# Kernel tuning notes

Measured on AMD Instinct MI355X. Metric: run time of the kernel, lower is better.

Reference implementation:

```python
import jax, jax.numpy as jnp
import numpy as np

N_NODES = 50000
N_EDGES = 1_600_000
IN_DIM = 256
OUT_DIM = 128
NEG_SLOPE = 0.01  # F.leaky_relu default


def setup_inputs() -> dict:
    key = jax.random.key(0)
    k1, k2, k3, k4, k5 = jax.random.split(key, 5)
    x = jax.random.normal(k1, (N_NODES, IN_DIM), dtype=jnp.float32)
    # glorot_init: uniform in [-r, r], r = sqrt(6/(in+out))
    r = np.sqrt(6.0 / (IN_DIM + OUT_DIM)).astype(np.float32)
    weight = jax.random.uniform(k2, (IN_DIM, OUT_DIM), dtype=jnp.float32, minval=-r, maxval=r)
    adj_rows = jax.random.randint(k3, (N_EDGES,), 0, N_NODES, dtype=jnp.int64 if jax.config.jax_enable_x64 else jnp.int32)
    adj_cols = jax.random.randint(k4, (N_EDGES,), 0, N_NODES, dtype=jnp.int64 if jax.config.jax_enable_x64 else jnp.int32)
    adj_vals = jax.random.uniform(k5, (N_EDGES,), dtype=jnp.float32)
    return {"x": x, "weight": weight, "adj_vals": adj_vals,
            "adj_rows": adj_rows, "adj_cols": adj_cols}


def reference(x, weight, adj_vals, adj_rows, adj_cols):
    # h = X @ W : [N, OUT_DIM]
    h = x @ weight
    # sparse adj @ h via edge-list SpMM: out[r] += v * h[c]
    msgs = adj_vals[:, None] * h[adj_cols]            # [E, OUT_DIM]
    agg = jax.ops.segment_sum(msgs, adj_rows, num_segments=N_NODES)
    # leaky_relu epilogue
    return jnp.where(agg >= 0, agg, NEG_SLOPE * agg)
```

## Files before the change

kernel.cpp:

```cpp
#include <hip/hip_runtime.h>
#include <hip/hip_fp16.h>

#define N_NODES 50000
#define N_EDGES 1600000
#define IN_DIM 256
#define OUT_DIM 128
#define NEG_SLOPE 0.01f

#define SB_SH     10
#define NSB       49
#define BIN_SH    4
#define BIN_ROWS  16
#define NBIN_PAD  (NSB * 64)
#define NPART     16
#define ECAP      2560
#define SEGP      96
#define CAPG      (NPART * SEGP)
#define OVF_CAP   65536

#define SCAT_BLOCKS 256
#define EPB_S (N_EDGES / SCAT_BLOCKS)
#define SCAT_ITERS ((EPB_S + 511) / 512)

#define BM 128
#define GEMM_BLOCKS ((N_NODES + BM - 1) / BM)
#define PREP_BLOCKS (SCAT_BLOCKS + GEMM_BLOCKS + 1)

typedef _Float16 f16x8 __attribute__((ext_vector_type(8)));
typedef float    f32x4 __attribute__((ext_vector_type(4)));
typedef float    f32x8 __attribute__((ext_vector_type(8)));

__device__ __forceinline__ float lrelu(float v) {
    return v >= 0.f ? v : NEG_SLOPE * v;
}

#define CVT16(lo, hi) do { \
    lo[0]=(_Float16)xr[0].x; lo[1]=(_Float16)xr[0].y; lo[2]=(_Float16)xr[0].z; lo[3]=(_Float16)xr[0].w; \
    lo[4]=(_Float16)xr[1].x; lo[5]=(_Float16)xr[1].y; lo[6]=(_Float16)xr[1].z; lo[7]=(_Float16)xr[1].w; \
    hi[0]=(_Float16)xr[2].x; hi[1]=(_Float16)xr[2].y; hi[2]=(_Float16)xr[2].z; hi[3]=(_Float16)xr[2].w; \
    hi[4]=(_Float16)xr[3].x; hi[5]=(_Float16)xr[3].y; hi[6]=(_Float16)xr[3].z; hi[7]=(_Float16)xr[3].w; \
} while (0)

__global__ __launch_bounds__(512, 2) void prep(const int* __restrict__ rows,
                                               const int* __restrict__ cols,
                                               const float* __restrict__ vals,
                                               const float* __restrict__ x,
                                               const float* __restrict__ w,
                                               int* __restrict__ cstartarr,
                                               int* __restrict__ ovfcnt,
                                               int2* __restrict__ cbuf,
                                               __half* __restrict__ h) {
    __shared__ __attribute__((aligned(16))) char smem[50432];
    const int bid = blockIdx.x;
    const int t   = threadIdx.x;

    if (bid >= SCAT_BLOCKS + GEMM_BLOCKS) {
        if (t == 0) *ovfcnt = 0;
        return;
    }

    if (bid < SCAT_BLOCKS) {
        int2* lsort  = (int2*)smem;
        int*  hist   = (int*)(smem + 50000);
        int*  cstart = (int*)(smem + 50200);
        const int lane  = t & 63;
        const int blk   = bid;
        const int ebase = blk * EPB_S;

        if (t < NSB) hist[t] = 0;
        __syncthreads();

        int myr[SCAT_ITERS];
#pragma unroll
        for (int k = 0; k < SCAT_ITERS; ++k) {
            const int i = k * 512 + t;
            myr[k] = -1;
            if (i < EPB_S) {
                myr[k] = rows[ebase + i];
                atomicAdd(&hist[myr[k] >> SB_SH], 1);
            }
        }
        __syncthreads();

        if (t < 64) {
            const int v = (t < NSB) ? hist[t] : 0;
            int s = v;
#pragma unroll
            for (int off = 1; off < 64; off <<= 1) {
                const int u = __shfl_up(s, off);
                if (lane >= off) s += u;
            }
            if (t < NSB) { cstart[t] = s - v; hist[t] = s - v; }
        }
        __syncthreads();

#pragma unroll
        for (int k = 0; k < SCAT_ITERS; ++k) {
            const int i = k * 512 + t;
            if (i < EPB_S) {
                const int e = ebase + i;
                const int r = myr[k];
                const int pos = atomicAdd(&hist[r >> SB_SH], 1);
                lsort[pos] = make_int2((int)(((unsigned)r << 16) | (unsigned)cols[e]),
                                       __float_as_int(vals[e]));
            }
        }
        __syncthreads();

        {
            const int4* src = (const int4*)lsort;
            int4* dst = (int4*)(cbuf + (size_t)blk * EPB_S);
            for (int i = t; i < EPB_S / 2; i += 512) dst[i] = src[i];
        }
        if (t < NSB)  cstartarr[blk * 50 + t]   = cstart[t];
        if (t == NSB) cstartarr[blk * 50 + NSB] = EPB_S;
        return;
    }

    f16x8* wt8h = (f16x8*)smem;
    f16x8* xs8  = (f16x8*)(smem + 32768);
    const int a256 = (t < 256);
    const int lane = t & 63;
    const int wv   = t >> 6;
    const int row0 = (bid - SCAT_BLOCKS) * BM;

    const int srow = t >> 1;
    const int skh  = t & 1;
    const int grow = row0 + srow;
    const bool rv  = a256 && (grow < N_NODES);
    const float* xp = x + (size_t)(rv ? grow : 0) * IN_DIM + skh * 16;

    float4 xr[4];
    if (a256) {
#pragma unroll
        for (int i = 0; i < 4; ++i)
            xr[i] = rv ? ((const float4*)xp)[i] : make_float4(0.f, 0.f, 0.f, 0.f);
        f16x8 lo, hi;
        CVT16(lo, hi);
        xs8[(0 * 4 + skh * 2 + 0) * 128 + srow] = lo;
        xs8[(0 * 4 + skh * 2 + 1) * 128 + srow] = hi;
    }
    __syncthreads();

    f32x4 acc[2][8];
#pragma unroll
    for (int mf = 0; mf < 2; ++mf)
#pragma unroll
        for (int nf = 0; nf < 8; ++nf) acc[mf][nf] = (f32x4){0.f, 0.f, 0.f, 0.f};

    const int kgl = lane >> 4;
    const int l15 = lane & 15;
    const int mb  = (wv << 5) + l15;

#pragma unroll
    for (int H = 0; H < 2; ++H) {
        if (a256) {
#pragma unroll
            for (int itr = 0; itr < 8; ++itr) {
                const int e  = itr * 2048 + t * 8;
                const int kl = e >> 7;
                const int n0 = e & 127;
                const float4 a4 = *(const float4*)(w + (size_t)((H << 7) + kl) * 128 + n0);
                const float4 b4 = *(const float4*)(w + (size_t)((H << 7) + kl) * 128 + n0 + 4);
                __half* d = (__half*)wt8h + (size_t)(((kl >> 3) << 7) + n0) * 8 + (kl & 7);
                d[0]  = __float2half(a4.x);
                d[8]  = __float2half(a4.y);
                d[16] = __float2half(a4.z);
                d[24] = __float2half(a4.w);
                d[32] = __float2half(b4.x);
                d[40] = __float2half(b4.y);
                d[48] = __float2half(b4.z);
                d[56] = __float2half(b4.w);
            }
        }
        __syncthreads();

#pragma unroll
        for (int ksl = 0; ksl < 4; ++ksl) {
            const int ks  = H * 4 + ksl;
            const int cur = ks & 1;
            if (a256 && ks < 7) {
#pragma unroll
                for (int i = 0; i < 4; ++i)
                    xr[i] = rv ? ((const float4*)(xp + (ks + 1) * 32))[i]
                               : make_float4(0.f, 0.f, 0.f, 0.f);
            }
            if (a256) {
                const f16x8 b0 = xs8[(cur * 4 + kgl) * 128 + mb];
                const f16x8 b1 = xs8[(cur * 4 + kgl) * 128 + mb + 16];
                const int abase = ((ksl * 4 + kgl) << 7) + l15;
#pragma unroll
                for (int nf = 0; nf < 8; ++nf) {
                    const f16x8 a = wt8h[abase + (nf << 4)];
                    acc[0][nf] = __builtin_amdgcn_mfma_f32_16x16x32_f16(a, b0, acc[0][nf], 0, 0, 0);
                    acc[1][nf] = __builtin_amdgcn_mfma_f32_16x16x32_f16(a, b1, acc[1][nf], 0, 0, 0);
                }
            }
            if (a256 && ks < 7) {
                f16x8 lo, hi;
                CVT16(lo, hi);
                xs8[((cur ^ 1) * 4 + skh * 2 + 0) * 128 + srow] = lo;
                xs8[((cur ^ 1) * 4 + skh * 2 + 1) * 128 + srow] = hi;
            }
            __syncthreads();
        }
    }

    if (a256) {
        const int rg = lane >> 4;
#pragma unroll
        for (int mf = 0; mf < 2; ++mf) {
            const int m = row0 + (wv << 5) + (mf << 4) + l15;
            if (m < N_NODES) {
                __half* hp = h + (size_t)m * OUT_DIM + (rg << 2);
#pragma unroll
                for (int nf = 0; nf < 8; ++nf) {
                    union { ushort4 u; __half f[4]; } o;
                    o.f[0] = __float2half(acc[mf][nf][0]);
                    o.f[1] = __float2half(acc[mf][nf][1]);
                    o.f[2] = __float2half(acc[mf][nf][2]);
                    o.f[3] = __float2half(acc[mf][nf][3]);
                    *(ushort4*)(hp + (nf << 4)) = o.u;
                }
            }
        }
    }
}

__global__ __launch_bounds__(512) void scatter_fine(const int* __restrict__ cstartarr,
                                                    int* __restrict__ fs,
                                                    int* __restrict__ fc,
                                                    int* __restrict__ ovfcnt,
                                                    const int2* __restrict__ cbuf,
                                                    int2* __restrict__ ebuf,
                                                    int2* __restrict__ ovfbuf) {
    __shared__ int2 lsort[ECAP];
    __shared__ int  hist[64], cstart[64], fcv[64];
    __shared__ int  scnt[16], sstart[16];
    __shared__ int  stot;

    const int t    = threadIdx.x;
    const int lane = t & 63;
    const int wv   = t >> 6;
    const int sb   = blockIdx.x / NPART;
    const int p    = blockIdx.x % NPART;

    if (t < 16) {
        const int blk = p * 16 + t;
        const int s0 = cstartarr[blk * 50 + sb];
        const int s1 = cstartarr[blk * 50 + sb + 1];
        scnt[t]   = s1 - s0;
        sstart[t] = blk * EPB_S + s0;
    }
    if (t < 64) hist[t] = 0;
    __syncthreads();

    for (int j = 0; j < 2; ++j) {
        const int s = (wv << 1) | j;
        const int c = scnt[s];
        const int base = sstart[s];
        for (int i = lane; i < c; i += 64)
            atomicAdd(&hist[((unsigned)cbuf[base + i].x >> 20) & 63], 1);
    }
    __syncthreads();

    if (t < 64) {
        const int v = hist[t];
        int s = v;
#pragma unroll
        for (int off = 1; off < 64; off <<= 1) {
            const int u = __shfl_up(s, off);
            if (t >= off) s += u;
        }
        if (t == 63) stot = s;
        cstart[t] = s - v;
        hist[t]   = s - v;
    }
    __syncthreads();

    for (int j = 0; j < 2; ++j) {
        const int s = (wv << 1) | j;
        const int c = scnt[s];
        const int base = sstart[s];
        for (int i = lane; i < c; i += 64) {
            const int2 rc = cbuf[base + i];
            const int fb = ((unsigned)rc.x >> 20) & 63;
            const int pos = atomicAdd(&hist[fb], 1);
            if (pos < ECAP) {
                lsort[pos] = rc;
            } else {
                const int q = atomicAdd(ovfcnt, 1);
                if (q < OVF_CAP) ovfbuf[q] = rc;
            }
        }
    }
    __syncthreads();

    if (t < 64) {
        int c = hist[t] - cstart[t];
        if (c > SEGP) c = SEGP;
        if (cstart[t] + c > ECAP) c = (cstart[t] < ECAP) ? (ECAP - cstart[t]) : 0;
        fcv[t] = c;
        fs[(sb * 64 + t) * NPART + p] = cstart[t];
        fc[(sb * 64 + t) * NPART + p] = c;
    }
    __syncthreads();

    const int tot = min(stot, ECAP);
    int2* dst = ebuf + (size_t)(sb * NPART + p) * ECAP;
    for (int i = t; i < tot; i += 512) {
        const int2 rc = lsort[i];
        dst[i] = rc;
        const int fb  = ((unsigned)rc.x >> 20) & 63;
        const int off = i - cstart[fb];
        if (off >= fcv[fb]) {
            const int q = atomicAdd(ovfcnt, 1);
            if (q < OVF_CAP) ovfbuf[q] = rc;
        }
    }
}

#define NCLS 256

__global__ __launch_bounds__(256) void sort_gather(const int* __restrict__ fs,
                                                   const int* __restrict__ fc,
                                                   const int* __restrict__ ovfcnt,
                                                   const int2* __restrict__ ebuf,
                                                   const int2* __restrict__ ovfbuf,
                                                   const __half* __restrict__ h,
                                                   float* __restrict__ out) {
    __shared__ int2 srec[CAPG];
    __shared__ int  hist[NCLS];
    __shared__ int  pfx[NCLS];
    __shared__ int  rowoff_l[BIN_ROWS + 1];
    __shared__ int  wsum[4];
    __shared__ int  poff[NPART + 1];
    __shared__ int  fsrt[NPART];

    const int t    = threadIdx.x;
    const int bin  = blockIdx.x;
    const int wv   = t >> 6;
    const int lane = t & 63;
    const int sb   = bin >> 6;

    hist[t] = 0;
    if (t < NPART) fsrt[t] = fs[bin * NPART + t];
    if (t == 0) {
        int a = 0;
        poff[0] = 0;
#pragma unroll
        for (int p = 0; p < NPART; ++p) { a += fc[bin * NPART + p]; poff[p + 1] = a; }
    }
    __syncthreads();
    const int cnt = poff[NPART];

#pragma unroll
    for (int j = 0; j < 4; ++j) {
        const int p  = (wv << 2) + j;
        const int cp = poff[p + 1] - poff[p];
        const int2* src = ebuf + (size_t)(sb * NPART + p) * ECAP + fsrt[p];
        for (int i = lane; i < cp; i += 64) {
            const int k = src[i].x;
            atomicAdd(&hist[(((k >> 16) & 15) << 4) | ((k & 0xFFFF) >> 12)], 1);
        }
    }
    __syncthreads();

    {
        const int v = hist[t];
        int s = v;
#pragma unroll
        for (int off = 1; off < 64; off <<= 1) {
            const int u = __shfl_up(s, off);
            if (lane >= off) s += u;
        }
        if (lane == 63) wsum[wv] = s;
        __syncthreads();
        if (t == 0) {
            int a = 0;
#pragma unroll
            for (int i = 0; i < 4; ++i) { const int c = wsum[i]; wsum[i] = a; a += c; }
        }
        __syncthreads();
        const int incl = s + wsum[wv];
        pfx[t]  = incl;
        hist[t] = incl - v;
    }
    __syncthreads();
    if (t < BIN_ROWS) rowoff_l[t] = t ? pfx[(t << 4) - 1] : 0;
    if (t == BIN_ROWS) rowoff_l[BIN_ROWS] = cnt;
    __syncthreads();

#pragma unroll
    for (int j = 0; j < 4; ++j) {
        const int p  = (wv << 2) + j;
        const int cp = poff[p + 1] - poff[p];
        const int2* src = ebuf + (size_t)(sb * NPART + p) * ECAP + fsrt[p];
        for (int i = lane; i < cp; i += 64) {
            const int2 r = src[i];
            const int cls = (((r.x >> 16) & 15) << 4) | ((r.x & 0xFFFF) >> 12);
            const int pos = atomicAdd(&hist[cls], 1);
            srec[pos] = r;
        }
    }
    __syncthreads();

    const int grp = lane >> 4;
    const int gl  = lane & 15;
    int novf = *ovfcnt;
    if (novf > OVF_CAP) novf = OVF_CAP;

    for (int pp = 0; pp < 2; ++pp) {
        const int lr0 = (wv << 2) + 2 * pp;
        const int lr1 = lr0 + 1;
        const int b0 = rowoff_l[lr0], e0 = rowoff_l[lr0 + 1];
        const int b1 = rowoff_l[lr1], e1 = rowoff_l[lr1 + 1];
        const int n0 = e0 - b0, n1 = e1 - b1;
        const int nmax = n0 > n1 ? n0 : n1;
        const int iters = (nmax + 3) >> 2;

        f32x8 a0 = (f32x8){0.f,0.f,0.f,0.f,0.f,0.f,0.f,0.f};
        f32x8 a1 = (f32x8){0.f,0.f,0.f,0.f,0.f,0.f,0.f,0.f};

        for (int it = 0; it < iters; ++it) {
            const int i0 = b0 + (it << 2) + grp;
            const int i1 = b1 + (it << 2) + grp;
            const bool v0i = i0 < e0;
            const bool v1i = i1 < e1;
            const int2 rA = srec[v0i ? i0 : 0];
            const int2 rB = srec[v1i ? i1 : 0];
            const float vA = v0i ? __int_as_float(rA.y) : 0.f;
            const float vB = v1i ? __int_as_float(rB.y) : 0.f;
            const f16x8 hA = *(const f16x8*)(h + (size_t)(rA.x & 0xFFFF) * OUT_DIM + (gl << 3));
            const f16x8 hB = *(const f16x8*)(h + (size_t)(rB.x & 0xFFFF) * OUT_DIM + (gl << 3));
#pragma unroll
            for (int j = 0; j < 8; ++j) {
                a0[j] += vA * (float)hA[j];
                a1[j] += vB * (float)hB[j];
            }
        }

        for (int e = 0; e < novf; ++e) {
            const int2 rec = ovfbuf[e];
            const unsigned urow = ((unsigned)rec.x) >> 16;
            if ((int)(urow >> BIN_SH) == bin && grp == 0) {
                const int lr = (int)(urow & (BIN_ROWS - 1));
                if (lr == lr0 || lr == lr1) {
                    const float v = __int_as_float(rec.y);
                    const f16x8 hv = *(const f16x8*)(h + (size_t)(rec.x & 0xFFFF) * OUT_DIM + (gl << 3));
#pragma unroll
                    for (int j = 0; j < 8; ++j) {
                        if (lr == lr0) a0[j] += v * (float)hv[j];
                        else           a1[j] += v * (float)hv[j];
                    }
                }
            }
        }

#pragma unroll
        for (int j = 0; j < 8; ++j) {
            float x0 = a0[j], x1 = a1[j];
            x0 += __shfl_xor(x0, 16); x0 += __shfl_xor(x0, 32);
            x1 += __shfl_xor(x1, 16); x1 += __shfl_xor(x1, 32);
            a0[j] = x0; a1[j] = x1;
        }

        const int lrow = (grp & 2) ? lr1 : lr0;
        const int grow = (bin << BIN_SH) + lrow;
        float q[4];
#pragma unroll
        for (int k = 0; k < 4; ++k) {
            const float lo = (grp & 2) ? a1[k]     : a0[k];
            const float hi = (grp & 2) ? a1[k + 4] : a0[k + 4];
            q[k] = lrelu((grp & 1) ? hi : lo);
        }
        if (grow < N_NODES) {
            float4 o = make_float4(q[0], q[1], q[2], q[3]);
            *(float4*)(out + (size_t)grow * OUT_DIM + (gl << 3) + ((grp & 1) << 2)) = o;
        }
    }
}

extern "C" void kernel_launch(void* const* d_in, const int* in_sizes, int n_in,
                              void* d_out, int out_size, void* d_ws, size_t ws_size,
                              hipStream_t stream) {
    const float* x    = (const float*)d_in[0];
    const float* w    = (const float*)d_in[1];
    const float* vals = (const float*)d_in[2];
    const int*   rows = (const int*)d_in[3];
    const int*   cols = (const int*)d_in[4];
    float* out = (float*)d_out;

    char* ws = (char*)d_ws;
    size_t off = 0;
    auto alloc = [&](size_t bytes) {
        void* p = ws + off;
        off = (off + bytes + 255) & ~(size_t)255;
        return p;
    };
    int2*   cbuf     = (int2*)  alloc((size_t)N_EDGES * sizeof(int2));
    __half* h        = (__half*)alloc((size_t)N_NODES * OUT_DIM * sizeof(__half));
    int2*   ebuf     = (int2*)  alloc((size_t)NSB * NPART * ECAP * sizeof(int2));
    int2*   ovfbuf   = (int2*)  alloc((size_t)OVF_CAP * sizeof(int2));
    int*    cstartarr= (int*)   alloc((size_t)SCAT_BLOCKS * 50 * sizeof(int));
    int*    fs       = (int*)   alloc((size_t)NBIN_PAD * NPART * sizeof(int));
    int*    fc       = (int*)   alloc((size_t)NBIN_PAD * NPART * sizeof(int));
    int*    ovfcnt   = (int*)   alloc(sizeof(int));

    prep<<<PREP_BLOCKS, 512, 0, stream>>>(rows, cols, vals, x, w,
                                          cstartarr, ovfcnt, cbuf, h);
    scatter_fine<<<NSB * NPART, 512, 0, stream>>>(cstartarr, fs, fc, ovfcnt,
                                                  cbuf, ebuf, ovfbuf);
    sort_gather<<<NBIN_PAD, 256, 0, stream>>>(fs, fc, ovfcnt, ebuf, ovfbuf, h, out);
}
```

Measured before the change: 192.5 us.

## Merge two-level edge binning into one fine-grained pass and drop scatter kernel

The coarse pass in prep now bins edges directly into 32-row classes (1563 bins) with a block-wide multi-wave prefix scan, replacing the 49 superbins. The intermediate scatter_fine kernel, its staging buffers and the overflow path are removed. sort_gather now takes one bin per block, reads each of the 256 producer segments straight from cbuf, sorts locally and accumulates 32 rows. This cuts a kernel launch and a full pass over the edge buffer. In exchange the per-segment reads in sort_gather are tiny, serial per thread and uncoalesced, the metadata table grows, and bins that exceed capacity fall back to a very slow serial path.

```diff
diff --git a/kernel.cpp b/kernel.cpp
--- a/kernel.cpp
+++ b/kernel.cpp
@@ -7,16 +7,12 @@
 #define OUT_DIM 128
 #define NEG_SLOPE 0.01f
 
-#define SB_SH     10
-#define NSB       49
-#define BIN_SH    4
-#define BIN_ROWS  16
-#define NBIN_PAD  (NSB * 64)
-#define NPART     16
-#define ECAP      2560
-#define SEGP      96
-#define CAPG      (NPART * SEGP)
-#define OVF_CAP   65536
+#define BIN_SH    5
+#define BIN_ROWS  32
+#define NCLASS    ((N_NODES + BIN_ROWS - 1) / BIN_ROWS)
+#define TSTRIDE   (NCLASS + 1)
+#define CAPG      1536
+#define NCLS      256
 
 #define SCAT_BLOCKS 256
 #define EPB_S (N_EDGES / SCAT_BLOCKS)
@@ -24,7 +20,7 @@
 
 #define BM 128
 #define GEMM_BLOCKS ((N_NODES + BM - 1) / BM)
-#define PREP_BLOCKS (SCAT_BLOCKS + GEMM_BLOCKS + 1)
+#define PREP_BLOCKS (SCAT_BLOCKS + GEMM_BLOCKS)
 
 typedef _Float16 f16x8 __attribute__((ext_vector_type(8)));
 typedef float    f32x4 __attribute__((ext_vector_type(4)));
@@ -47,27 +43,23 @@
                                                const float* __restrict__ x,
                                                const float* __restrict__ w,
                                                int* __restrict__ cstartarr,
-                                               int* __restrict__ ovfcnt,
                                                int2* __restrict__ cbuf,
                                                __half* __restrict__ h) {
-    __shared__ __attribute__((aligned(16))) char smem[50432];
+    __shared__ __attribute__((aligned(16))) char smem[62560];
     const int bid = blockIdx.x;
     const int t   = threadIdx.x;
-
-    if (bid >= SCAT_BLOCKS + GEMM_BLOCKS) {
-        if (t == 0) *ovfcnt = 0;
-        return;
-    }
 
     if (bid < SCAT_BLOCKS) {
         int2* lsort  = (int2*)smem;
         int*  hist   = (int*)(smem + 50000);
-        int*  cstart = (int*)(smem + 50200);
+        int*  cstart = (int*)(smem + 56256);
+        int*  wsum8  = (int*)(smem + 62512);
         const int lane  = t & 63;
+        const int wv    = t >> 6;
         const int blk   = bid;
         const int ebase = blk * EPB_S;
 
-        if (t < NSB) hist[t] = 0;
+        for (int m = t; m < NCLASS; m += 512) hist[m] = 0;
         __syncthreads();
 
         int myr[SCAT_ITERS];
@@ -77,20 +69,37 @@
             myr[k] = -1;
             if (i < EPB_S) {
                 myr[k] = rows[ebase + i];
-                atomicAdd(&hist[myr[k] >> SB_SH], 1);
-            }
-        }
-        __syncthreads();
-
-        if (t < 64) {
-            const int v = (t < NSB) ? hist[t] : 0;
-            int s = v;
+                atomicAdd(&hist[myr[k] >> BIN_SH], 1);
+            }
+        }
+        __syncthreads();
+
+        {
+            const int base = t << 2;
+            const int v0 = (base + 0 < NCLASS) ? hist[base + 0] : 0;
+            const int v1 = (base + 1 < NCLASS) ? hist[base + 1] : 0;
+            const int v2 = (base + 2 < NCLASS) ? hist[base + 2] : 0;
+            const int v3 = (base + 3 < NCLASS) ? hist[base + 3] : 0;
+            const int sum = v0 + v1 + v2 + v3;
+            int s = sum;
 #pragma unroll
             for (int off = 1; off < 64; off <<= 1) {
                 const int u = __shfl_up(s, off);
                 if (lane >= off) s += u;
             }
-            if (t < NSB) { cstart[t] = s - v; hist[t] = s - v; }
+            if (lane == 63) wsum8[wv] = s;
+            __syncthreads();
+            if (t == 0) {
+                int a = 0;
+#pragma unroll
+                for (int i = 0; i < 8; ++i) { const int c = wsum8[i]; wsum8[i] = a; a += c; }
+            }
+            __syncthreads();
+            const int excl = s - sum + wsum8[wv];
+            if (base + 0 < NCLASS) { cstart[base + 0] = excl;               hist[base + 0] = excl; }
+            if (base + 1 < NCLASS) { cstart[base + 1] = excl + v0;          hist[base + 1] = excl + v0; }
+            if (base + 2 < NCLASS) { cstart[base + 2] = excl + v0 + v1;     hist[base + 2] = excl + v0 + v1; }
+            if (base + 3 < NCLASS) { cstart[base + 3] = excl + v0 + v1 + v2; hist[base + 3] = excl + v0 + v1 + v2; }
         }
         __syncthreads();
 
@@ -100,7 +109,7 @@
             if (i < EPB_S) {
                 const int e = ebase + i;
                 const int r = myr[k];
-                const int pos = atomicAdd(&hist[r >> SB_SH], 1);
+                const int pos = atomicAdd(&hist[r >> BIN_SH], 1);
                 lsort[pos] = make_int2((int)(((unsigned)r << 16) | (unsigned)cols[e]),
                                        __float_as_int(vals[e]));
             }
@@ -112,8 +121,8 @@
             int4* dst = (int4*)(cbuf + (size_t)blk * EPB_S);
             for (int i = t; i < EPB_S / 2; i += 512) dst[i] = src[i];
         }
-        if (t < NSB)  cstartarr[blk * 50 + t]   = cstart[t];
-        if (t == NSB) cstartarr[blk * 50 + NSB] = EPB_S;
+        for (int m = t; m < NCLASS; m += 512) cstartarr[blk * TSTRIDE + m] = cstart[m];
+        if (t == 0) cstartarr[blk * TSTRIDE + NCLASS] = EPB_S;
         return;
     }
 
@@ -227,256 +236,171 @@
     }
 }
 
-__global__ __launch_bounds__(512) void scatter_fine(const int* __restrict__ cstartarr,
-                                                    int* __restrict__ fs,
-                                                    int* __restrict__ fc,
-                                                    int* __restrict__ ovfcnt,
-                                                    const int2* __restrict__ cbuf,
-                                                    int2* __restrict__ ebuf,
-                                                    int2* __restrict__ ovfbuf) {
-    __shared__ int2 lsort[ECAP];
-    __shared__ int  hist[64], cstart[64], fcv[64];
-    __shared__ int  scnt[16], sstart[16];
-    __shared__ int  stot;
-
-    const int t    = threadIdx.x;
-    const int lane = t & 63;
-    const int wv   = t >> 6;
-    const int sb   = blockIdx.x / NPART;
-    const int p    = blockIdx.x % NPART;
-
-    if (t < 16) {
-        const int blk = p * 16 + t;
-        const int s0 = cstartarr[blk * 50 + sb];
-        const int s1 = cstartarr[blk * 50 + sb + 1];
-        scnt[t]   = s1 - s0;
-        sstart[t] = blk * EPB_S + s0;
-    }
-    if (t < 64) hist[t] = 0;
-    __syncthreads();
-
-    for (int j = 0; j < 2; ++j) {
-        const int s = (wv << 1) | j;
-        const int c = scnt[s];
-        const int base = sstart[s];
-        for (int i = lane; i < c; i += 64)
-            atomicAdd(&hist[((unsigned)cbuf[base + i].x >> 20) & 63], 1);
-    }
-    __syncthreads();
-
-    if (t < 64) {
-        const int v = hist[t];
-        int s = v;
-#pragma unroll
-        for (int off = 1; off < 64; off <<= 1) {
-            const int u = __shfl_up(s, off);
-            if (t >= off) s += u;
-        }
-        if (t == 63) stot = s;
-        cstart[t] = s - v;
-        hist[t]   = s - v;
-    }
-    __syncthreads();
-
-    for (int j = 0; j < 2; ++j) {
-        const int s = (wv << 1) | j;
-        const int c = scnt[s];
-        const int base = sstart[s];
-        for (int i = lane; i < c; i += 64) {
-            const int2 rc = cbuf[base + i];
-            const int fb = ((unsigned)rc.x >> 20) & 63;
-            const int pos = atomicAdd(&hist[fb], 1);
-            if (pos < ECAP) {
-                lsort[pos] = rc;
-            } else {
-                const int q = atomicAdd(ovfcnt, 1);
-                if (q < OVF_CAP) ovfbuf[q] = rc;
-            }
-        }
-    }
-    __syncthreads();
-
-    if (t < 64) {
-        int c = hist[t] - cstart[t];
-        if (c > SEGP) c = SEGP;
-        if (cstart[t] + c > ECAP) c = (cstart[t] < ECAP) ? (ECAP - cstart[t]) : 0;
-        fcv[t] = c;
-        fs[(sb * 64 + t) * NPART + p] = cstart[t];
-        fc[(sb * 64 + t) * NPART + p] = c;
-    }
-    __syncthreads();
-
-    const int tot = min(stot, ECAP);
-    int2* dst = ebuf + (size_t)(sb * NPART + p) * ECAP;
-    for (int i = t; i < tot; i += 512) {
-        const int2 rc = lsort[i];
-        dst[i] = rc;
-        const int fb  = ((unsigned)rc.x >> 20) & 63;
-        const int off = i - cstart[fb];
-        if (off >= fcv[fb]) {
-            const int q = atomicAdd(ovfcnt, 1);
-            if (q < OVF_CAP) ovfbuf[q] = rc;
-        }
-    }
-}
-
-#define NCLS 256
-
-__global__ __launch_bounds__(256) void sort_gather(const int* __restrict__ fs,
-                                                   const int* __restrict__ fc,
-                                                   const int* __restrict__ ovfcnt,
-                                                   const int2* __restrict__ ebuf,
-                                                   const int2* __restrict__ ovfbuf,
+#define GCLS(K) ((((K) >> 16) & 31) << 3 | (((K) & 0xFFFF) >> 13))
+
+__global__ __launch_bounds__(256) void sort_gather(const int* __restrict__ cstartarr,
+                                                   const int2* __restrict__ cbuf,
                                                    const __half* __restrict__ h,
                                                    float* __restrict__ out) {
+    __shared__ int2 urec[CAPG];
     __shared__ int2 srec[CAPG];
     __shared__ int  hist[NCLS];
-    __shared__ int  pfx[NCLS];
     __shared__ int  rowoff_l[BIN_ROWS + 1];
     __shared__ int  wsum[4];
-    __shared__ int  poff[NPART + 1];
-    __shared__ int  fsrt[NPART];
+    __shared__ int  cnt_sh;
 
     const int t    = threadIdx.x;
     const int bin  = blockIdx.x;
     const int wv   = t >> 6;
     const int lane = t & 63;
-    const int sb   = bin >> 6;
 
     hist[t] = 0;
-    if (t < NPART) fsrt[t] = fs[bin * NPART + t];
+
+    const int s0 = cstartarr[t * TSTRIDE + bin];
+    const int c  = cstartarr[t * TSTRIDE + bin + 1] - s0;
+
+    int s = c;
+#pragma unroll
+    for (int off = 1; off < 64; off <<= 1) {
+        const int u = __shfl_up(s, off);
+        if (lane >= off) s += u;
+    }
+    if (lane == 63) wsum[wv] = s;
+    __syncthreads();
     if (t == 0) {
         int a = 0;
-        poff[0] = 0;
-#pragma unroll
-        for (int p = 0; p < NPART; ++p) { a += fc[bin * NPART + p]; poff[p + 1] = a; }
+#pragma unroll
+        for (int i = 0; i < 4; ++i) { const int q = wsum[i]; wsum[i] = a; a += q; }
+        cnt_sh = a;
     }
     __syncthreads();
-    const int cnt = poff[NPART];
-
-#pragma unroll
-    for (int j = 0; j < 4; ++j) {
-        const int p  = (wv << 2) + j;
-        const int cp = poff[p + 1] - poff[p];
-        const int2* src = ebuf + (size_t)(sb * NPART + p) * ECAP + fsrt[p];
-        for (int i = lane; i < cp; i += 64) {
-            const int k = src[i].x;
-            atomicAdd(&hist[(((k >> 16) & 15) << 4) | ((k & 0xFFFF) >> 12)], 1);
-        }
-    }
-    __syncthreads();
-
-    {
-        const int v = hist[t];
-        int s = v;
-#pragma unroll
-        for (int off = 1; off < 64; off <<= 1) {
-            const int u = __shfl_up(s, off);
-            if (lane >= off) s += u;
-        }
-        if (lane == 63) wsum[wv] = s;
-        __syncthreads();
-        if (t == 0) {
-            int a = 0;
-#pragma unroll
-            for (int i = 0; i < 4; ++i) { const int c = wsum[i]; wsum[i] = a; a += c; }
-        }
-        __syncthreads();
-        const int incl = s + wsum[wv];
-        pfx[t]  = incl;
-        hist[t] = incl - v;
-    }
-    __syncthreads();
-    if (t < BIN_ROWS) rowoff_l[t] = t ? pfx[(t << 4) - 1] : 0;
-    if (t == BIN_ROWS) rowoff_l[BIN_ROWS] = cnt;
-    __syncthreads();
-
-#pragma unroll
-    for (int j = 0; j < 4; ++j) {
-        const int p  = (wv << 2) + j;
-        const int cp = poff[p + 1] - poff[p];
-        const int2* src = ebuf + (size_t)(sb * NPART + p) * ECAP + fsrt[p];
-        for (int i = lane; i < cp; i += 64) {
+    const int excl = s - c + wsum[wv];
+    const int cnt  = cnt_sh;
+
+    if (cnt <= CAPG) {
+        const int2* src = cbuf + (size_t)t * EPB_S + s0;
+        for (int i = 0; i < c; ++i) {
             const int2 r = src[i];
-            const int cls = (((r.x >> 16) & 15) << 4) | ((r.x & 0xFFFF) >> 12);
-            const int pos = atomicAdd(&hist[cls], 1);
+            urec[excl + i] = r;
+            atomicAdd(&hist[GCLS(r.x)], 1);
+        }
+        __syncthreads();
+
+        {
+            const int v = hist[t];
+            int ss = v;
+#pragma unroll
+            for (int off = 1; off < 64; off <<= 1) {
+                const int u = __shfl_up(ss, off);
+                if (lane >= off) ss += u;
+            }
+            if (lane == 63) wsum[wv] = ss;
+            __syncthreads();
+            if (t == 0) {
+                int a = 0;
+#pragma unroll
+                for (int i = 0; i < 4; ++i) { const int q = wsum[i]; wsum[i] = a; a += q; }
+            }
+            __syncthreads();
+            hist[t] = ss + wsum[wv] - v;
+        }
+        __syncthreads();
+        if (t < BIN_ROWS) rowoff_l[t] = hist[t << 3];
+        if (t == 0) rowoff_l[BIN_ROWS] = cnt;
+        __syncthreads();
+
+        for (int i = t; i < cnt; i += 256) {
+            const int2 r = urec[i];
+            const int pos = atomicAdd(&hist[GCLS(r.x)], 1);
             srec[pos] = r;
         }
-    }
-    __syncthreads();
-
-    const int grp = lane >> 4;
-    const int gl  = lane & 15;
-    int novf = *ovfcnt;
-    if (novf > OVF_CAP) novf = OVF_CAP;
-
-    for (int pp = 0; pp < 2; ++pp) {
-        const int lr0 = (wv << 2) + 2 * pp;
-        const int lr1 = lr0 + 1;
-        const int b0 = rowoff_l[lr0], e0 = rowoff_l[lr0 + 1];
-        const int b1 = rowoff_l[lr1], e1 = rowoff_l[lr1 + 1];
-        const int n0 = e0 - b0, n1 = e1 - b1;
-        const int nmax = n0 > n1 ? n0 : n1;
-        const int iters = (nmax + 3) >> 2;
-
-        f32x8 a0 = (f32x8){0.f,0.f,0.f,0.f,0.f,0.f,0.f,0.f};
-        f32x8 a1 = (f32x8){0.f,0.f,0.f,0.f,0.f,0.f,0.f,0.f};
-
-        for (int it = 0; it < iters; ++it) {
-            const int i0 = b0 + (it << 2) + grp;
-            const int i1 = b1 + (it << 2) + grp;
-            const bool v0i = i0 < e0;
-            const bool v1i = i1 < e1;
-            const int2 rA = srec[v0i ? i0 : 0];
-            const int2 rB = srec[v1i ? i1 : 0];
-            const float vA = v0i ? __int_as_float(rA.y) : 0.f;
-            const float vB = v1i ? __int_as_float(rB.y) : 0.f;
-            const f16x8 hA = *(const f16x8*)(h + (size_t)(rA.x & 0xFFFF) * OUT_DIM + (gl << 3));
-            const f16x8 hB = *(const f16x8*)(h + (size_t)(rB.x & 0xFFFF) * OUT_DIM + (gl << 3));
+        __syncthreads();
+
+        const int grp = lane >> 4;
+        const int gl  = lane & 15;
+
+        for (int pp = 0; pp < 4; ++pp) {
+            const int lr0 = (wv << 3) + 2 * pp;
+            const int lr1 = lr0 + 1;
+            const int b0 = rowoff_l[lr0], e0 = rowoff_l[lr0 + 1];
+            const int b1 = rowoff_l[lr1], e1 = rowoff_l[lr1 + 1];
+            const int n0 = e0 - b0, n1 = e1 - b1;
+            const int nmax = n0 > n1 ? n0 : n1;
+            const int iters = (nmax + 3) >> 2;
+
+            f32x8 a0 = (f32x8){0.f,0.f,0.f,0.f,0.f,0.f,0.f,0.f};
+            f32x8 a1 = (f32x8){0.f,0.f,0.f,0.f,0.f,0.f,0.f,0.f};
+
+            for (int it = 0; it < iters; ++it) {
+                const int i0 = b0 + (it << 2) + grp;
+                const int i1 = b1 + (it << 2) + grp;
+                const bool v0i = i0 < e0;
+                const bool v1i = i1 < e1;
+                const int2 rA = srec[v0i ? i0 : 0];
+                const int2 rB = srec[v1i ? i1 : 0];
+                const float vA = v0i ? __int_as_float(rA.y) : 0.f;
+                const float vB = v1i ? __int_as_float(rB.y) : 0.f;
+                const f16x8 hA = *(const f16x8*)(h + (size_t)(rA.x & 0xFFFF) * OUT_DIM + (gl << 3));
+                const f16x8 hB = *(const f16x8*)(h + (size_t)(rB.x & 0xFFFF) * OUT_DIM + (gl << 3));
+#pragma unroll
+                for (int j = 0; j < 8; ++j) {
+                    a0[j] += vA * (float)hA[j];
+                    a1[j] += vB * (float)hB[j];
+                }
+            }
+
 #pragma unroll
             for (int j = 0; j < 8; ++j) {
-                a0[j] += vA * (float)hA[j];
-                a1[j] += vB * (float)hB[j];
-            }
-        }
-
-        for (int e = 0; e < novf; ++e) {
-            const int2 rec = ovfbuf[e];
-            const unsigned urow = ((unsigned)rec.x) >> 16;
-            if ((int)(urow >> BIN_SH) == bin && grp == 0) {
-                const int lr = (int)(urow & (BIN_ROWS - 1));
-                if (lr == lr0 || lr == lr1) {
-                    const float v = __int_as_float(rec.y);
-                    const f16x8 hv = *(const f16x8*)(h + (size_t)(rec.x & 0xFFFF) * OUT_DIM + (gl << 3));
-#pragma unroll
-                    for (int j = 0; j < 8; ++j) {
-                        if (lr == lr0) a0[j] += v * (float)hv[j];
-                        else           a1[j] += v * (float)hv[j];
+                float x0 = a0[j], x1 = a1[j];
+                x0 += __shfl_xor(x0, 16); x0 += __shfl_xor(x0, 32);
+                x1 += __shfl_xor(x1, 16); x1 += __shfl_xor(x1, 32);
+                a0[j] = x0; a1[j] = x1;
+            }
+
+            const int lrow = (grp & 2) ? lr1 : lr0;
+            const int grow = (bin << BIN_SH) + lrow;
+            float q[4];
+#pragma unroll
+            for (int k = 0; k < 4; ++k) {
+                const float lo = (grp & 2) ? a1[k]     : a0[k];
+                const float hi = (grp & 2) ? a1[k + 4] : a0[k + 4];
+                q[k] = lrelu((grp & 1) ? hi : lo);
+            }
+            if (grow < N_NODES) {
+                float4 o = make_float4(q[0], q[1], q[2], q[3]);
+                *(float4*)(out + (size_t)grow * OUT_DIM + (gl << 3) + ((grp & 1) << 2)) = o;
+            }
+        }
+    } else {
+        for (int pp = 0; pp < 4; ++pp) {
+            const int lr0 = (wv << 3) + 2 * pp;
+            const int lr1 = lr0 + 1;
+            float2 a0 = make_float2(0.f, 0.f);
+            float2 a1 = make_float2(0.f, 0.f);
+            for (int b = 0; b < 256; ++b) {
+                const int sb = cstartarr[b * TSTRIDE + bin];
+                const int eb = cstartarr[b * TSTRIDE + bin + 1];
+                for (int e = sb; e < eb; ++e) {
+                    const int2 rec = cbuf[(size_t)b * EPB_S + e];
+                    const int lr = (rec.x >> 16) & 31;
+                    if (lr == lr0 || lr == lr1) {
+                        const float v = __int_as_float(rec.y);
+                        const float2 m = __half22float2(((const __half2*)(h + (size_t)(rec.x & 0xFFFF) * OUT_DIM))[lane]);
+                        if (lr == lr0) { a0.x += v * m.x; a0.y += v * m.y; }
+                        else           { a1.x += v * m.x; a1.y += v * m.y; }
                     }
                 }
             }
-        }
-
-#pragma unroll
-        for (int j = 0; j < 8; ++j) {
-            float x0 = a0[j], x1 = a1[j];
-            x0 += __shfl_xor(x0, 16); x0 += __shfl_xor(x0, 32);
-            x1 += __shfl_xor(x1, 16); x1 += __shfl_xor(x1, 32);
-            a0[j] = x0; a1[j] = x1;
-        }
-
-        const int lrow = (grp & 2) ? lr1 : lr0;
-        const int grow = (bin << BIN_SH) + lrow;
-        float q[4];
-#pragma unroll
-        for (int k = 0; k < 4; ++k) {
-            const float lo = (grp & 2) ? a1[k]     : a0[k];
-            const float hi = (grp & 2) ? a1[k + 4] : a0[k + 4];
-            q[k] = lrelu((grp & 1) ? hi : lo);
-        }
-        if (grow < N_NODES) {
-            float4 o = make_float4(q[0], q[1], q[2], q[3]);
-            *(float4*)(out + (size_t)grow * OUT_DIM + (gl << 3) + ((grp & 1) << 2)) = o;
+            const int g0 = (bin << BIN_SH) + lr0;
+            const int g1 = (bin << BIN_SH) + lr1;
+            if (g0 < N_NODES) {
+                float2 o = make_float2(lrelu(a0.x), lrelu(a0.y));
+                ((float2*)(out + (size_t)g0 * OUT_DIM))[lane] = o;
+            }
+            if (g1 < N_NODES) {
+                float2 o = make_float2(lrelu(a1.x), lrelu(a1.y));
+                ((float2*)(out + (size_t)g1 * OUT_DIM))[lane] = o;
+            }
         }
     }
 }
@@ -500,16 +424,8 @@
     };
     int2*   cbuf     = (int2*)  alloc((size_t)N_EDGES * sizeof(int2));
     __half* h        = (__half*)alloc((size_t)N_NODES * OUT_DIM * sizeof(__half));
-    int2*   ebuf     = (int2*)  alloc((size_t)NSB * NPART * ECAP * sizeof(int2));
-    int2*   ovfbuf   = (int2*)  alloc((size_t)OVF_CAP * sizeof(int2));
-    int*    cstartarr= (int*)   alloc((size_t)SCAT_BLOCKS * 50 * sizeof(int));
-    int*    fs       = (int*)   alloc((size_t)NBIN_PAD * NPART * sizeof(int));
-    int*    fc       = (int*)   alloc((size_t)NBIN_PAD * NPART * sizeof(int));
-    int*    ovfcnt   = (int*)   alloc(sizeof(int));
-
-    prep<<<PREP_BLOCKS, 512, 0, stream>>>(rows, cols, vals, x, w,
-                                          cstartarr, ovfcnt, cbuf, h);
-    scatter_fine<<<NSB * NPART, 512, 0, stream>>>(cstartarr, fs, fc, ovfcnt,
-                                                  cbuf, ebuf, ovfbuf);
-    sort_gather<<<NBIN_PAD, 256, 0, stream>>>(fs, fc, ovfcnt, ebuf, ovfbuf, h, out);
+    int*    cstartarr= (int*)   alloc((size_t)SCAT_BLOCKS * TSTRIDE * sizeof(int));
+
+    prep<<<PREP_BLOCKS, 512, 0, stream>>>(rows, cols, vals, x, w, cstartarr, cbuf, h);
+    sort_gather<<<NCLASS, 256, 0, stream>>>(cstartarr, cbuf, h, out);
 }
```

Result: slower. 205.8 us (+6.9%).
